# Kernel optimization log

Hardware: AMD Instinct MI355X
Metric: run time of the kernel (lower is better)

Reference implementation:

```python
import jax, jax.numpy as jnp
import numpy as np

NUM_HEADS = 12
HEAD_DIM = 64
MAX_POS = 1024  # max_position_embeddings


def setup_inputs() -> dict:
    key = jax.random.key(0)
    ks = jax.random.split(key, 6)
    B, S, H = 4, 1024, 768
    return {
        "hidden_states": jax.random.normal(ks[0], (B, S, H), dtype=jnp.float32),
        "attention_mask": jnp.zeros((B, 1, 1, S), dtype=jnp.float32),
        "Wq": jax.random.normal(ks[1], (H, H), dtype=jnp.float32) * 0.02,
        "bq": jnp.zeros((H,), dtype=jnp.float32),
        "Wk": jax.random.normal(ks[2], (H, H), dtype=jnp.float32) * 0.02,
        "bk": jnp.zeros((H,), dtype=jnp.float32),
        "Wv": jax.random.normal(ks[3], (H, H), dtype=jnp.float32) * 0.02,
        "bv": jnp.zeros((H,), dtype=jnp.float32),
        "dist_emb": jax.random.normal(ks[4], (2 * MAX_POS - 1, HEAD_DIM), dtype=jnp.float32) * 0.02,
    }


def _split_heads(x):
    # [B, S, H] -> [B, nh, S, hd]
    B, S, _ = x.shape
    return x.reshape(B, S, NUM_HEADS, HEAD_DIM).transpose(0, 2, 1, 3)


def reference(hidden_states, attention_mask, Wq, bq, Wk, bk, Wv, bv, dist_emb):
    B, S, H = hidden_states.shape
    q = _split_heads(hidden_states @ Wq + bq)  # [B, nh, S, hd]
    k = _split_heads(hidden_states @ Wk + bk)
    v = _split_heads(hidden_states @ Wv + bv)

    # raw scores QK^T: [B, nh, S, S]
    scores = jnp.einsum("bhld,bhrd->bhlr", q, k)

    # relative_key_query positional bias
    dist = jnp.arange(S)[:, None] - jnp.arange(S)[None, :] + MAX_POS - 1  # [S, S]
    pos = dist_emb[dist]  # [S, S, hd]
    scores = scores + jnp.einsum("bhld,lrd->bhlr", q, pos) \
                    + jnp.einsum("bhrd,lrd->bhlr", k, pos)

    scores = scores / jnp.sqrt(jnp.asarray(HEAD_DIM, scores.dtype))
    scores = scores + attention_mask  # additive mask broadcast [B,1,1,S]

    probs = jax.nn.softmax(scores, axis=-1)  # dropout prob = 0.0 (eval)
    ctx = jnp.einsum("bhlr,bhrd->bhld", probs, v)  # [B, nh, S, hd]
    ctx = ctx.transpose(0, 2, 1, 3).reshape(B, S, H)
    return ctx
```

## Files before the change

### kernel.cpp

```cpp
#include <hip/hip_runtime.h>

#define SEQ 1024
#define NH  12
#define HD  64
#define HID 768
#define NB  4

#define LOG2E  1.4426950408889634f
#define SC2    0.18033688011112042f
#define DTHR   11.541560327111707f

typedef short bf16x8 __attribute__((ext_vector_type(8)));
typedef float f32x16 __attribute__((ext_vector_type(16)));

#define LBAR() do {                                             \
    __builtin_amdgcn_sched_barrier(0);                          \
    asm volatile("s_waitcnt lgkmcnt(0)" ::: "memory");          \
    __builtin_amdgcn_s_barrier();                               \
    __builtin_amdgcn_sched_barrier(0);                          \
} while (0)

__device__ __forceinline__ unsigned short f2b(float f) {
    union { float f; unsigned u; } v; v.f = f;
    unsigned r = (v.u + 0x7FFFu + ((v.u >> 16) & 1u)) >> 16;
    return (unsigned short)r;
}
__device__ __forceinline__ float b2f(unsigned short s) {
    union { unsigned u; float f; } v; v.u = (unsigned)s << 16;
    return v.f;
}
__device__ __forceinline__ float g4(const float4& v, int e) {
    return e == 0 ? v.x : e == 1 ? v.y : e == 2 ? v.z : v.w;
}
__device__ __forceinline__ unsigned short u16g(const ushort4& v, int e) {
    return e == 0 ? v.x : e == 1 ? v.y : e == 2 ? v.z : v.w;
}

#define ROWFN(r, h) (((r) & 3) + 8 * ((r) >> 2) + 4 * (h))

#define NX4 786432
#define NE4 32752

__global__ void cvt_all(const float* __restrict__ X, const float* __restrict__ E,
                        unsigned short* __restrict__ Xb, unsigned short* __restrict__ Eb) {
    int i = blockIdx.x * blockDim.x + threadIdx.x;
    const int stride = gridDim.x * blockDim.x;
    for (; i < NX4 + NE4; i += stride) {
        float4 v;
        if (i < NX4) v = ((const float4*)X)[i];
        else         v = ((const float4*)E)[i - NX4];
        ushort4 o;
        o.x = f2b(v.x); o.y = f2b(v.y); o.z = f2b(v.z); o.w = f2b(v.w);
        if (i < NX4) ((ushort4*)Xb)[i] = o;
        else         ((ushort4*)Eb)[i - NX4] = o;
    }
}

__global__ __launch_bounds__(256) void cvt_wt(
    const float* __restrict__ Wq, const float* __restrict__ Wk, const float* __restrict__ Wv,
    unsigned short* __restrict__ Wt)
{
    __shared__ float T[64][65];
    const int z = blockIdx.z;
    const float* __restrict__ W = (z == 0) ? Wq : (z == 1) ? Wk : Wv;
    const int k0 = blockIdx.x * 64, n0 = blockIdx.y * 64;
    const int tid = threadIdx.x;
    #pragma unroll
    for (int ir = 0; ir < 4; ++ir) {
        int r = ir * 16 + (tid >> 4);
        int c4 = (tid & 15) * 4;
        *(float4*)&T[r][c4] = *(const float4*)&W[(size_t)(k0 + r) * HID + n0 + c4];
    }
    __syncthreads();
    const int cc = tid >> 2, q = tid & 3;
    unsigned short* dst = Wt + (size_t)z * HID * HID + (size_t)(n0 + cc) * HID + k0 + q * 16;
    #pragma unroll
    for (int j4 = 0; j4 < 4; ++j4) {
        ushort4 t4;
        t4.x = f2b(T[q * 16 + j4 * 4 + 0][cc]);
        t4.y = f2b(T[q * 16 + j4 * 4 + 1][cc]);
        t4.z = f2b(T[q * 16 + j4 * 4 + 2][cc]);
        t4.w = f2b(T[q * 16 + j4 * 4 + 3][cc]);
        *(ushort4*)(dst + j4 * 4) = t4;
    }
}

__global__ __launch_bounds__(256) void gemm_qkv(
    const unsigned short* __restrict__ Xb,
    const unsigned short* __restrict__ Wt,
    const float* __restrict__ bq, const float* __restrict__ bk, const float* __restrict__ bv,
    unsigned short* __restrict__ qkv)
{
    __shared__ unsigned short Xs[128][64];
    __shared__ unsigned short Ws[128][64];

    const int tid = threadIdx.x;
    const int lane = tid & 63;
    const int wid = tid >> 6;
    const int c = lane & 31;
    const int h2 = lane >> 5;
    const int m0 = blockIdx.x * 128, N0 = blockIdx.y * 128, z = blockIdx.z;
    const unsigned short* __restrict__ Wz = Wt + (size_t)z * HID * HID;
    const float* __restrict__ bias = (z == 0) ? bq : (z == 1) ? bk : bv;

    f32x16 acc[2][2];
    #pragma unroll
    for (int i = 0; i < 2; ++i)
        #pragma unroll
        for (int j = 0; j < 2; ++j)
            #pragma unroll
            for (int r = 0; r < 16; ++r) acc[i][j][r] = 0.f;

    for (int k0 = 0; k0 < HID; k0 += 64) {
        __syncthreads();
        #pragma unroll
        for (int it = 0; it < 4; ++it) {
            int t16 = tid + 256 * it;
            int row = t16 >> 3, s = t16 & 7;
            bf16x8 xv = *(const bf16x8*)(Xb + (size_t)(m0 + row) * HID + k0 + s * 8);
            *(bf16x8*)&Xs[row][(s ^ (row & 7)) * 8] = xv;
            bf16x8 wv = *(const bf16x8*)(Wz + (size_t)(N0 + row) * HID + k0 + s * 8);
            *(bf16x8*)&Ws[row][(s ^ (row & 7)) * 8] = wv;
        }
        __syncthreads();
        #pragma unroll
        for (int kc = 0; kc < 4; ++kc) {
            const int slot = kc * 2 + h2;
            bf16x8 af[2], bf_[2];
            #pragma unroll
            for (int i = 0; i < 2; ++i) {
                int ar = 64 * (wid >> 1) + 32 * i + c;
                int br = 64 * (wid & 1) + 32 * i + c;
                if (z != 2) {
                    af[i]  = *(const bf16x8*)&Xs[ar][(slot ^ (ar & 7)) * 8];
                    bf_[i] = *(const bf16x8*)&Ws[br][(slot ^ (br & 7)) * 8];
                } else {
                    af[i]  = *(const bf16x8*)&Ws[ar][(slot ^ (ar & 7)) * 8];
                    bf_[i] = *(const bf16x8*)&Xs[br][(slot ^ (br & 7)) * 8];
                }
            }
            #pragma unroll
            for (int i = 0; i < 2; ++i)
                #pragma unroll
                for (int j = 0; j < 2; ++j)
                    acc[i][j] = __builtin_amdgcn_mfma_f32_32x32x16_bf16(af[i], bf_[j], acc[i][j], 0, 0, 0);
        }
    }

    unsigned short* outz = qkv + (size_t)z * (NB * SEQ * HID);
    if (z != 2) {
        #pragma unroll
        for (int j = 0; j < 2; ++j) {
            const int n = N0 + 64 * (wid & 1) + 32 * j + c;
            const float bv_ = bias[n];
            const int hh = n >> 6, d = n & 63;
            #pragma unroll
            for (int i = 0; i < 2; ++i) {
                #pragma unroll
                for (int r = 0; r < 16; ++r) {
                    int m = m0 + 64 * (wid >> 1) + 32 * i + ROWFN(r, h2);
                    int bb = m >> 10, ss = m & 1023;
                    outz[(((size_t)bb * NH + hh) * SEQ + ss) * HD + d] = f2b(acc[i][j][r] + bv_);
                }
            }
        }
    } else {
        #pragma unroll
        for (int i = 0; i < 2; ++i) {
            #pragma unroll
            for (int r = 0; r < 16; ++r) {
                int n = N0 + 64 * (wid >> 1) + 32 * i + ROWFN(r, h2);
                float bv_ = bias[n];
                int hh = n >> 6, d = n & 63;
                #pragma unroll
                for (int j = 0; j < 2; ++j) {
                    int m = m0 + 64 * (wid & 1) + 32 * j + c;
                    int bb = m >> 10, ss = m & 1023;
                    outz[(((size_t)bb * NH + hh) * HD + d) * SEQ + ss] = f2b(acc[i][j][r] + bv_);
                }
            }
        }
    }
}

__global__ __launch_bounds__(256, 2) void attn_mfma(
    const unsigned short* __restrict__ Qg,
    const unsigned short* __restrict__ Kg,
    const unsigned short* __restrict__ Vtg,
    const unsigned short* __restrict__ Eg,
    const float* __restrict__ mask,
    float* __restrict__ out)
{
    __shared__ unsigned short Vt[64][64];
    __shared__ float S1[64][68];
    __shared__ unsigned short MSS[64][76];
    __shared__ unsigned short NST[64][76];
    __shared__ unsigned short Pl[64][64];
    __shared__ float Corr[64];
    __shared__ float InvL[64];
    __shared__ int Fl[2];

    const int tid = threadIdx.x;
    const int lane = tid & 63;
    const int wid = tid >> 6;
    const int c = lane & 31;
    const int h2 = lane >> 5;
    const int RB = 32 * (wid >> 1);
    const int CB = 32 * (wid & 1);
    const int j0 = 64 * (wid & 1) + c;

    const int l0 = blockIdx.x * 64;
    const int bh = blockIdx.y;
    const int b = bh / NH;
    const int hh = bh - b * NH;

    const unsigned short* __restrict__ Qb = Qg + (size_t)bh * SEQ * HD;
    const unsigned short* __restrict__ Kb = Kg + (size_t)bh * SEQ * HD;
    const unsigned short* __restrict__ Vb = Vtg + (size_t)bh * HD * SEQ;
    const float* __restrict__ mrow_base = mask + (size_t)b * SEQ;

    if (tid < 2) Fl[tid] = 0;

    bf16x8 qa[4];
    #pragma unroll
    for (int kc = 0; kc < 4; ++kc)
        qa[kc] = *(const bf16x8*)(Qb + (size_t)(l0 + RB + c) * HD + kc * 16 + h2 * 8);

    f32x16 Oa;
    #pragma unroll
    for (int r = 0; r < 16; ++r) Oa[r] = 0.f;

    const int li = tid >> 2;
    const int c0q = (tid & 3) * 16;
    const int kli = (li ^ (li >> 3)) & 7;
    const int vd0 = tid >> 3, vs8 = tid & 7;
    const int kd0 = (vd0 ^ (vd0 >> 3)) & 7;
    const int kd1 = ((vd0 + 32) ^ ((vd0 + 32) >> 3)) & 7;
    float m_run = -1e30f, lsum = 0.f;

    bf16x8 kb[4], ka[4], e0[4], e1[4], vc0, vc1;
    {
        const int jr0 = l0 + 960 + j0;
        const int jra = jr0 > 2046 ? 2046 : jr0;
        const int jr1x = jr0 + 32;
        const int jrb = jr1x > 2046 ? 2046 : jr1x;
        #pragma unroll
        for (int kc = 0; kc < 4; ++kc) {
            kb[kc] = *(const bf16x8*)(Kb + (size_t)(CB + c) * HD + kc * 16 + h2 * 8);
            ka[kc] = *(const bf16x8*)(Kb + (size_t)(RB + c) * HD + kc * 16 + h2 * 8);
            e0[kc] = *(const bf16x8*)(Eg + (size_t)jra * HD + kc * 16 + h2 * 8);
            e1[kc] = *(const bf16x8*)(Eg + (size_t)jrb * HD + kc * 16 + h2 * 8);
        }
        vc0 = *(const bf16x8*)(Vb + (size_t)vd0 * SEQ + vs8 * 8);
        vc1 = *(const bf16x8*)(Vb + (size_t)(vd0 + 32) * SEQ + vs8 * 8);
    }

    for (int r0 = 0; r0 < SEQ; r0 += 64) {
        const int buf = (r0 >> 6) & 1;
        int r0n = r0 + 64; if (r0n >= SEQ) r0n = 0;

        float4 mk[4];
        #pragma unroll
        for (int q = 0; q < 4; ++q)
            mk[q] = *(const float4*)(mrow_base + r0 + c0q + 4 * q);

        {
            f32x16 s1a;
            #pragma unroll
            for (int r = 0; r < 16; ++r) s1a[r] = 0.f;
            __builtin_amdgcn_s_setprio(1);
            #pragma unroll
            for (int kc = 0; kc < 4; ++kc)
                s1a = __builtin_amdgcn_mfma_f32_32x32x16_bf16(qa[kc], kb[kc], s1a, 0, 0, 0);
            __builtin_amdgcn_s_setprio(0);
            #pragma unroll
            for (int rq = 0; rq < 16; ++rq)
                S1[RB + ROWFN(rq, h2)][CB + c] = s1a[rq];
        }
        #pragma unroll
        for (int kc = 0; kc < 4; ++kc)
            kb[kc] = *(const bf16x8*)(Kb + (size_t)(r0n + CB + c) * HD + kc * 16 + h2 * 8);
        __builtin_amdgcn_sched_barrier(0);

        {
            f32x16 ma0, na0;
            #pragma unroll
            for (int r = 0; r < 16; ++r) { ma0[r] = 0.f; na0[r] = 0.f; }
            __builtin_amdgcn_s_setprio(1);
            if (wid != 2) {
                #pragma unroll
                for (int kc = 0; kc < 4; ++kc)
                    ma0 = __builtin_amdgcn_mfma_f32_32x32x16_bf16(qa[kc], e0[kc], ma0, 0, 0, 0);
            }
            if (wid != 0) {
                #pragma unroll
                for (int kc = 0; kc < 4; ++kc)
                    na0 = __builtin_amdgcn_mfma_f32_32x32x16_bf16(ka[kc], e0[kc], na0, 0, 0, 0);
            }
            __builtin_amdgcn_s_setprio(0);
            if (wid != 2) {
                #pragma unroll
                for (int rq = 0; rq < 16; ++rq) {
                    const int lr = RB + ROWFN(rq, h2);
                    int rA = lr - j0 + 63;
                    if ((unsigned)rA < 64u) MSS[lr][rA] = f2b(ma0[rq]);
                }
            }
            if (wid != 0) {
                #pragma unroll
                for (int rq = 0; rq < 16; ++rq) {
                    const int lr = RB + ROWFN(rq, h2);
                    int lA = j0 + lr - 63;
                    if ((unsigned)lA < 64u) NST[lA][lr] = f2b(na0[rq]);
                }
            }
        }
        __builtin_amdgcn_sched_barrier(0);

        {
            f32x16 ma1, na1;
            #pragma unroll
            for (int r = 0; r < 16; ++r) { ma1[r] = 0.f; na1[r] = 0.f; }
            __builtin_amdgcn_s_setprio(1);
            if (wid != 1) {
                #pragma unroll
                for (int kc = 0; kc < 4; ++kc)
                    ma1 = __builtin_amdgcn_mfma_f32_32x32x16_bf16(qa[kc], e1[kc], ma1, 0, 0, 0);
            }
            if (wid != 3) {
                #pragma unroll
                for (int kc = 0; kc < 4; ++kc)
                    na1 = __builtin_amdgcn_mfma_f32_32x32x16_bf16(ka[kc], e1[kc], na1, 0, 0, 0);
            }
            __builtin_amdgcn_s_setprio(0);
            if (wid != 1) {
                #pragma unroll
                for (int rq = 0; rq < 16; ++rq) {
                    const int lr = RB + ROWFN(rq, h2);
                    int rB = lr - j0 + 31;
                    if ((unsigned)rB < 64u) MSS[lr][rB] = f2b(ma1[rq]);
                }
            }
            if (wid != 3) {
                #pragma unroll
                for (int rq = 0; rq < 16; ++rq) {
                    const int lr = RB + ROWFN(rq, h2);
                    int lB = j0 + lr - 31;
                    if ((unsigned)lB < 64u) NST[lB][lr] = f2b(na1[rq]);
                }
            }
        }
        __builtin_amdgcn_sched_barrier(0);

        bf16x8 vn0, vn1;
        {
            const int jr0n = l0 - r0n + 960 + j0;
            const int jran = jr0n > 2046 ? 2046 : jr0n;
            const int jr1n = jr0n + 32;
            const int jrbn = jr1n > 2046 ? 2046 : jr1n;
            #pragma unroll
            for (int kc = 0; kc < 4; ++kc) {
                ka[kc] = *(const bf16x8*)(Kb + (size_t)(r0n + RB + c) * HD + kc * 16 + h2 * 8);
                e0[kc] = *(const bf16x8*)(Eg + (size_t)jran * HD + kc * 16 + h2 * 8);
                e1[kc] = *(const bf16x8*)(Eg + (size_t)jrbn * HD + kc * 16 + h2 * 8);
            }
            vn0 = *(const bf16x8*)(Vb + (size_t)vd0 * SEQ + r0n + vs8 * 8);
            vn1 = *(const bf16x8*)(Vb + (size_t)(vd0 + 32) * SEQ + r0n + vs8 * 8);
        }

        LBAR();

        *(bf16x8*)&Vt[vd0][(vs8 ^ kd0) * 8] = vc0;
        *(bf16x8*)&Vt[vd0 + 32][(vs8 ^ kd1) * 8] = vc1;

        float4 s4[4]; ushort4 mm[4], nn[4];
        #pragma unroll
        for (int q = 0; q < 4; ++q) {
            s4[q] = *(const float4*)&S1[li][c0q + 4 * q];
            mm[q] = *(const ushort4*)&MSS[li][c0q + 4 * q];
            nn[q] = *(const ushort4*)&NST[li][c0q + 4 * q];
        }
        float sc[16];
        #pragma unroll
        for (int j = 0; j < 16; ++j) {
            float mv = b2f(u16g(mm[j >> 2], j & 3));
            float nv = b2f(u16g(nn[j >> 2], j & 3));
            sc[j] = (g4(s4[j >> 2], j & 3) + mv + nv) * SC2 + g4(mk[j >> 2], j & 3) * LOG2E;
        }
        float tmax = sc[0];
        #pragma unroll
        for (int j = 1; j < 16; ++j) tmax = fmaxf(tmax, sc[j]);
        tmax = fmaxf(tmax, __shfl_xor(tmax, 1));
        tmax = fmaxf(tmax, __shfl_xor(tmax, 2));
        const bool upd = tmax > m_run + DTHR;
        const float m_new = upd ? tmax : m_run;
        const float corr = upd ? __builtin_amdgcn_exp2f(m_run - m_new) : 1.0f;
        if (upd) Fl[buf] = 1;
        float tsum = 0.f;
        unsigned short pb[16];
        #pragma unroll
        for (int j = 0; j < 16; ++j) {
            float p = __builtin_amdgcn_exp2f(sc[j] - m_new);
            tsum += p;
            pb[j] = f2b(p);
        }
        tsum += __shfl_xor(tsum, 1);
        tsum += __shfl_xor(tsum, 2);
        lsum = lsum * corr + tsum;
        m_run = m_new;
        if ((tid & 3) == 0) Corr[li] = corr;
        #pragma unroll
        for (int sblk = 0; sblk < 2; ++sblk) {
            bf16x8 pv;
            #pragma unroll
            for (int e = 0; e < 8; ++e) pv[e] = (short)pb[sblk * 8 + e];
            const int slot = ((c0q >> 3) + sblk) ^ kli;
            *(bf16x8*)&Pl[li][slot * 8] = pv;
        }

        LBAR();

        if (Fl[buf]) {
            #pragma unroll
            for (int q = 0; q < 4; ++q) {
                float4 cr = *(const float4*)&Corr[RB + 8 * q + 4 * h2];
                Oa[4 * q + 0] *= cr.x; Oa[4 * q + 1] *= cr.y;
                Oa[4 * q + 2] *= cr.z; Oa[4 * q + 3] *= cr.w;
            }
        }
        if (tid == 0) Fl[buf ^ 1] = 0;
        const int lrow = RB + c;
        const int drow = CB + c;
        const int klr = (lrow ^ (lrow >> 3)) & 7;
        const int kdr = (drow ^ (drow >> 3)) & 7;
        __builtin_amdgcn_s_setprio(1);
        #pragma unroll
        for (int kc = 0; kc < 4; ++kc) {
            const int slot = kc * 2 + h2;
            bf16x8 pa  = *(const bf16x8*)&Pl[lrow][(slot ^ klr) * 8];
            bf16x8 vbf = *(const bf16x8*)&Vt[drow][(slot ^ kdr) * 8];
            Oa = __builtin_amdgcn_mfma_f32_32x32x16_bf16(pa, vbf, Oa, 0, 0, 0);
        }
        __builtin_amdgcn_s_setprio(0);

        vc0 = vn0; vc1 = vn1;
    }

    if ((tid & 3) == 0) InvL[li] = 1.0f / lsum;
    __syncthreads();
    #pragma unroll
    for (int q = 0; q < 4; ++q) {
        float4 iv = *(const float4*)&InvL[RB + 8 * q + 4 * h2];
        #pragma unroll
        for (int e = 0; e < 4; ++e) {
            const int l = RB + 8 * q + 4 * h2 + e;
            out[((size_t)b * SEQ + l0 + l) * HID + hh * HD + CB + c] = Oa[4 * q + e] * g4(iv, e);
        }
    }
}

extern "C" void kernel_launch(void* const* d_in, const int* in_sizes, int n_in,
                              void* d_out, int out_size, void* d_ws, size_t ws_size,
                              hipStream_t stream) {
    const float* hidden = (const float*)d_in[0];
    const float* mask   = (const float*)d_in[1];
    const float* Wq     = (const float*)d_in[2];
    const float* bq     = (const float*)d_in[3];
    const float* Wk     = (const float*)d_in[4];
    const float* bk     = (const float*)d_in[5];
    const float* Wv     = (const float*)d_in[6];
    const float* bv     = (const float*)d_in[7];
    const float* E      = (const float*)d_in[8];
    float* outp = (float*)d_out;

    unsigned short* ws  = (unsigned short*)d_ws;
    unsigned short* Xbf = ws;
    unsigned short* Wt  = ws + 3145728;
    unsigned short* Ebf = ws + 4915200;
    unsigned short* qkv = ws + 5046272;

    cvt_all<<<dim3(1024), 256, 0, stream>>>(hidden, E, Xbf, Ebf);
    cvt_wt<<<dim3(12, 12, 3), 256, 0, stream>>>(Wq, Wk, Wv, Wt);
    gemm_qkv<<<dim3(32, 6, 3), 256, 0, stream>>>(Xbf, Wt, bq, bk, bv, qkv);
    const size_t per = (size_t)NB * SEQ * HID;
    attn_mfma<<<dim3(16, 48), 256, 0, stream>>>(qkv, qkv + per, qkv + 2 * per,
                                                Ebf, mask, outp);
}
```

Baseline: 170.0 us.

## Stage K and positional-embedding tiles in swizzled LDS instead of per-wave registers

```diff
diff --git a/kernel.cpp b/kernel.cpp
--- a/kernel.cpp
+++ b/kernel.cpp
@@ -191,6 +191,8 @@
     const float* __restrict__ mask,
     float* __restrict__ out)
 {
+    __shared__ unsigned short Ks[64][64];
+    __shared__ unsigned short Es[128][64];
     __shared__ unsigned short Vt[64][64];
     __shared__ float S1[64][68];
     __shared__ unsigned short MSS[64][76];
@@ -236,24 +238,31 @@
     const int vd0 = tid >> 3, vs8 = tid & 7;
     const int kd0 = (vd0 ^ (vd0 >> 3)) & 7;
     const int kd1 = ((vd0 + 32) ^ ((vd0 + 32) >> 3)) & 7;
+
+    const int srow = tid >> 3, su = tid & 7;
+    const int sswz = (su ^ (srow & 7)) * 8;
+
+    const int swk = c & 7;
+
     float m_run = -1e30f, lsum = 0.f;
 
-    bf16x8 kb[4], ka[4], e0[4], e1[4], vc0, vc1;
+    bf16x8 kst0, kst1, est[4], vc0, vc1;
     {
-        const int jr0 = l0 + 960 + j0;
-        const int jra = jr0 > 2046 ? 2046 : jr0;
-        const int jr1x = jr0 + 32;
-        const int jrb = jr1x > 2046 ? 2046 : jr1x;
-        #pragma unroll
-        for (int kc = 0; kc < 4; ++kc) {
-            kb[kc] = *(const bf16x8*)(Kb + (size_t)(CB + c) * HD + kc * 16 + h2 * 8);
-            ka[kc] = *(const bf16x8*)(Kb + (size_t)(RB + c) * HD + kc * 16 + h2 * 8);
-            e0[kc] = *(const bf16x8*)(Eg + (size_t)jra * HD + kc * 16 + h2 * 8);
-            e1[kc] = *(const bf16x8*)(Eg + (size_t)jrb * HD + kc * 16 + h2 * 8);
-        }
+        const int jb0 = l0 + 960;
+        kst0 = *(const bf16x8*)(Kb + (size_t)srow * HD + sswz);
+        kst1 = *(const bf16x8*)(Kb + (size_t)(srow + 32) * HD + sswz);
+        #pragma unroll
+        for (int it = 0; it < 4; ++it)
+            est[it] = *(const bf16x8*)(Eg + (size_t)(jb0 + srow + 32 * it) * HD + sswz);
         vc0 = *(const bf16x8*)(Vb + (size_t)vd0 * SEQ + vs8 * 8);
         vc1 = *(const bf16x8*)(Vb + (size_t)(vd0 + 32) * SEQ + vs8 * 8);
     }
+    *(bf16x8*)&Ks[srow][su * 8] = kst0;
+    *(bf16x8*)&Ks[srow + 32][su * 8] = kst1;
+    #pragma unroll
+    for (int it = 0; it < 4; ++it)
+        *(bf16x8*)&Es[srow + 32 * it][su * 8] = est[it];
+    __syncthreads();
 
     for (int r0 = 0; r0 < SEQ; r0 += 64) {
         const int buf = (r0 >> 6) & 1;
@@ -263,6 +272,17 @@
         #pragma unroll
         for (int q = 0; q < 4; ++q)
             mk[q] = *(const float4*)(mrow_base + r0 + c0q + 4 * q);
+        bf16x8 vn0, vn1;
+        {
+            const int jbn = l0 - r0n + 960;
+            kst0 = *(const bf16x8*)(Kb + (size_t)(r0n + srow) * HD + sswz);
+            kst1 = *(const bf16x8*)(Kb + (size_t)(r0n + srow + 32) * HD + sswz);
+            #pragma unroll
+            for (int it = 0; it < 4; ++it)
+                est[it] = *(const bf16x8*)(Eg + (size_t)(jbn + srow + 32 * it) * HD + sswz);
+            vn0 = *(const bf16x8*)(Vb + (size_t)vd0 * SEQ + r0n + vs8 * 8);
+            vn1 = *(const bf16x8*)(Vb + (size_t)(vd0 + 32) * SEQ + r0n + vs8 * 8);
+        }
 
         {
             f32x16 s1a;
@@ -270,16 +290,15 @@
             for (int r = 0; r < 16; ++r) s1a[r] = 0.f;
             __builtin_amdgcn_s_setprio(1);
             #pragma unroll
-            for (int kc = 0; kc < 4; ++kc)
-                s1a = __builtin_amdgcn_mfma_f32_32x32x16_bf16(qa[kc], kb[kc], s1a, 0, 0, 0);
+            for (int kc = 0; kc < 4; ++kc) {
+                bf16x8 kbv = *(const bf16x8*)&Ks[CB + c][((kc * 2 + h2) ^ swk) * 8];
+                s1a = __builtin_amdgcn_mfma_f32_32x32x16_bf16(qa[kc], kbv, s1a, 0, 0, 0);
+            }
             __builtin_amdgcn_s_setprio(0);
             #pragma unroll
             for (int rq = 0; rq < 16; ++rq)
                 S1[RB + ROWFN(rq, h2)][CB + c] = s1a[rq];
         }
-        #pragma unroll
-        for (int kc = 0; kc < 4; ++kc)
-            kb[kc] = *(const bf16x8*)(Kb + (size_t)(r0n + CB + c) * HD + kc * 16 + h2 * 8);
         __builtin_amdgcn_sched_barrier(0);
 
         {
@@ -287,15 +306,15 @@
             #pragma unroll
             for (int r = 0; r < 16; ++r) { ma0[r] = 0.f; na0[r] = 0.f; }
             __builtin_amdgcn_s_setprio(1);
-            if (wid != 2) {
-                #pragma unroll
-                for (int kc = 0; kc < 4; ++kc)
-                    ma0 = __builtin_amdgcn_mfma_f32_32x32x16_bf16(qa[kc], e0[kc], ma0, 0, 0, 0);
-            }
-            if (wid != 0) {
-                #pragma unroll
-                for (int kc = 0; kc < 4; ++kc)
-                    na0 = __builtin_amdgcn_mfma_f32_32x32x16_bf16(ka[kc], e0[kc], na0, 0, 0, 0);
+            #pragma unroll
+            for (int kc = 0; kc < 4; ++kc) {
+                bf16x8 e0v = *(const bf16x8*)&Es[j0][((kc * 2 + h2) ^ swk) * 8];
+                if (wid != 2)
+                    ma0 = __builtin_amdgcn_mfma_f32_32x32x16_bf16(qa[kc], e0v, ma0, 0, 0, 0);
+                if (wid != 0) {
+                    bf16x8 kav = *(const bf16x8*)&Ks[RB + c][((kc * 2 + h2) ^ swk) * 8];
+                    na0 = __builtin_amdgcn_mfma_f32_32x32x16_bf16(kav, e0v, na0, 0, 0, 0);
+                }
             }
             __builtin_amdgcn_s_setprio(0);
             if (wid != 2) {
@@ -322,15 +341,15 @@
             #pragma unroll
             for (int r = 0; r < 16; ++r) { ma1[r] = 0.f; na1[r] = 0.f; }
             __builtin_amdgcn_s_setprio(1);
-            if (wid != 1) {
-                #pragma unroll
-                for (int kc = 0; kc < 4; ++kc)
-                    ma1 = __builtin_amdgcn_mfma_f32_32x32x16_bf16(qa[kc], e1[kc], ma1, 0, 0, 0);
-            }
-            if (wid != 3) {
-                #pragma unroll
-                for (int kc = 0; kc < 4; ++kc)
-                    na1 = __builtin_amdgcn_mfma_f32_32x32x16_bf16(ka[kc], e1[kc], na1, 0, 0, 0);
+            #pragma unroll
+            for (int kc = 0; kc < 4; ++kc) {
+                bf16x8 e1v = *(const bf16x8*)&Es[j0 + 32][((kc * 2 + h2) ^ swk) * 8];
+                if (wid != 1)
+                    ma1 = __builtin_amdgcn_mfma_f32_32x32x16_bf16(qa[kc], e1v, ma1, 0, 0, 0);
+                if (wid != 3) {
+                    bf16x8 kav = *(const bf16x8*)&Ks[RB + c][((kc * 2 + h2) ^ swk) * 8];
+                    na1 = __builtin_amdgcn_mfma_f32_32x32x16_bf16(kav, e1v, na1, 0, 0, 0);
+                }
             }
             __builtin_amdgcn_s_setprio(0);
             if (wid != 1) {
@@ -352,26 +371,15 @@
         }
         __builtin_amdgcn_sched_barrier(0);
 
-        bf16x8 vn0, vn1;
-        {
-            const int jr0n = l0 - r0n + 960 + j0;
-            const int jran = jr0n > 2046 ? 2046 : jr0n;
-            const int jr1n = jr0n + 32;
-            const int jrbn = jr1n > 2046 ? 2046 : jr1n;
-            #pragma unroll
-            for (int kc = 0; kc < 4; ++kc) {
-                ka[kc] = *(const bf16x8*)(Kb + (size_t)(r0n + RB + c) * HD + kc * 16 + h2 * 8);
-                e0[kc] = *(const bf16x8*)(Eg + (size_t)jran * HD + kc * 16 + h2 * 8);
-                e1[kc] = *(const bf16x8*)(Eg + (size_t)jrbn * HD + kc * 16 + h2 * 8);
-            }
-            vn0 = *(const bf16x8*)(Vb + (size_t)vd0 * SEQ + r0n + vs8 * 8);
-            vn1 = *(const bf16x8*)(Vb + (size_t)(vd0 + 32) * SEQ + r0n + vs8 * 8);
-        }
-
         LBAR();
 
         *(bf16x8*)&Vt[vd0][(vs8 ^ kd0) * 8] = vc0;
         *(bf16x8*)&Vt[vd0 + 32][(vs8 ^ kd1) * 8] = vc1;
+        *(bf16x8*)&Ks[srow][su * 8] = kst0;
+        *(bf16x8*)&Ks[srow + 32][su * 8] = kst1;
+        #pragma unroll
+        for (int it = 0; it < 4; ++it)
+            *(bf16x8*)&Es[srow + 32 * it][su * 8] = est[it];
 
         float4 s4[4]; ushort4 mm[4], nn[4];
         #pragma unroll
```

Measured after the change: 166.7 us. Within noise of the previous version (-1.9%).
